# Optimization experiments

Hardware: AMD Instinct MI355X
Metric: run time of the kernel (lower is better)

Reference implementation:

```python
import jax, jax.numpy as jnp
import numpy as np


def _glorot(key, shape):
    fan_in, fan_out = shape[0], shape[1]
    lim = np.sqrt(6.0 / (fan_in + fan_out))
    return jax.random.uniform(key, shape, jnp.float32, -lim, lim)


def setup_inputs() -> dict:
    key = jax.random.key(0)
    ks = jax.random.split(key, 32)
    B, NR, NT = 16384, 64, 128
    inp = {
        "tier0_features": jax.random.normal(ks[0], (B, 44), jnp.float32),
        "robot_features": jax.random.normal(ks[1], (B, NR, 6), jnp.float32),
        "track_features": jax.random.normal(ks[2], (B, NT, 7), jnp.float32),
        # robot SetEncoder: 6 -> 64 -> 64 -> 32
        "rw1": _glorot(ks[3], (6, 64)),  "rb1": jnp.zeros((64,), jnp.float32),
        "rw2": _glorot(ks[4], (64, 64)), "rb2": jnp.zeros((64,), jnp.float32),
        "rw3": _glorot(ks[5], (64, 32)), "rb3": jnp.zeros((32,), jnp.float32),
        # track SetEncoder: 7 -> 64 -> 64 -> 32
        "tw1": _glorot(ks[6], (7, 64)),  "tb1": jnp.zeros((64,), jnp.float32),
        "tw2": _glorot(ks[7], (64, 64)), "tb2": jnp.zeros((64,), jnp.float32),
        "tw3": _glorot(ks[8], (64, 32)), "tb3": jnp.zeros((32,), jnp.float32),
        # head MLP: 108 -> 128 -> 128 -> 64 -> 1
        "mw1": _glorot(ks[9], (108, 128)),  "mb1": jnp.zeros((128,), jnp.float32),
        "mw2": _glorot(ks[10], (128, 128)), "mb2": jnp.zeros((128,), jnp.float32),
        "mw3": _glorot(ks[11], (128, 64)),  "mb3": jnp.zeros((64,), jnp.float32),
        "mw4": _glorot(ks[12], (64, 1)),    "mb4": jnp.zeros((1,), jnp.float32),
    }
    return inp


def _set_encode(x, w1, b1, w2, b2, w3, b3):
    # x: [B, N, d_in] -> pooled [B, 32]; mask=None path: mean+max over set dim
    h = jax.nn.relu(jnp.einsum('bnd,dh->bnh', x, w1) + b1)
    h = jax.nn.relu(jnp.einsum('bnh,hk->bnk', h, w2) + b2)
    e = jnp.einsum('bnk,ko->bno', h, w3) + b3
    return (e.mean(axis=1) + e.max(axis=1)) * 0.5


def reference(tier0_features, robot_features, track_features,
              rw1, rb1, rw2, rb2, rw3, rb3,
              tw1, tb1, tw2, tb2, tw3, tb3,
              mw1, mb1, mw2, mb2, mw3, mb3, mw4, mb4):
    robot_emb = _set_encode(robot_features, rw1, rb1, rw2, rb2, rw3, rb3)  # [B,32]
    track_emb = _set_encode(track_features, tw1, tb1, tw2, tb2, tw3, tb3)  # [B,32]
    c = jnp.concatenate([tier0_features, robot_emb, track_emb], axis=1)    # [B,108]
    h = jax.nn.relu(c @ mw1 + mb1)
    h = jax.nn.relu(h @ mw2 + mb2)
    h = jax.nn.relu(h @ mw3 + mb3)
    return (h @ mw4 + mb4).squeeze(-1)  # [B]
```

## Files before the change

kernel.cpp:

```cpp
#include <hip/hip_runtime.h>
#include <hip/hip_bf16.h>

#define DEV_INLINE __device__ __forceinline__

typedef __bf16 bf16x8 __attribute__((ext_vector_type(8)));
typedef float  floatx4 __attribute__((ext_vector_type(4)));

DEV_INLINE bf16x8 ld_frag(const __bf16* p) {
    union { uint4 u; bf16x8 v; } t;
    t.u = *(const uint4*)p;
    return t.v;
}
DEV_INLINE bf16x8 pack_relu2(floatx4 a, floatx4 b) {
    float2 p0 = {fmaxf(a[0], 0.0f), fmaxf(a[1], 0.0f)};
    float2 p1 = {fmaxf(a[2], 0.0f), fmaxf(a[3], 0.0f)};
    float2 p2 = {fmaxf(b[0], 0.0f), fmaxf(b[1], 0.0f)};
    float2 p3 = {fmaxf(b[2], 0.0f), fmaxf(b[3], 0.0f)};
    union { __hip_bfloat162 h[4]; bf16x8 v; } t;
    t.h[0] = __float22bfloat162_rn(p0);
    t.h[1] = __float22bfloat162_rn(p1);
    t.h[2] = __float22bfloat162_rn(p2);
    t.h[3] = __float22bfloat162_rn(p3);
    return t.v;
}
DEV_INLINE floatx4 vmax4(floatx4 a, floatx4 b) {
    floatx4 r;
#pragma unroll
    for (int i = 0; i < 4; ++i) r[i] = fmaxf(a[i], b[i]);
    return r;
}

template<int N, int Kp, int Ks>
DEV_INLINE void tp(__bf16* dst, const float* __restrict__ src, int idx0, int stride) {
    for (int e = idx0; e < N * Kp; e += stride) {
        int n = e / Kp, k = e - n * Kp;
        dst[e] = (k < Ks) ? (__bf16)src[k * N + n] : (__bf16)0.0f;
    }
}
template<int N, int Kp, int Ks>
DEV_INLINE void tp_b(__bf16* dst, const float* __restrict__ src,
                     const float* __restrict__ bias, int idx0, int stride) {
    for (int e = idx0; e < N * Kp; e += stride) {
        int n = e / Kp, k = e - n * Kp;
        float v = (k < Ks) ? src[k * N + n] : ((k == Ks) ? bias[n] : 0.0f);
        dst[e] = (__bf16)v;
    }
}
template<int N, int K>
DEV_INLINE void tp_perm(__bf16* dst, const float* __restrict__ src, int idx0, int stride) {
    for (int e = idx0; e < N * K; e += stride) {
        int n = e / K, kh = e - n * K;
        int qd = (kh >> 3) & 3, kq = kh >> 5, j = kh & 7;
        int c = (2 * kq + (j >> 2)) * 16 + qd * 4 + (j & 3);
        dst[e] = (__bf16)src[c * N + n];
    }
}

__global__ __launch_bounds__(256)
void prep_kernel(const float* __restrict__ rw1, const float* __restrict__ rb1,
                 const float* __restrict__ rw2, const float* __restrict__ rw3,
                 const float* __restrict__ tw1, const float* __restrict__ tb1,
                 const float* __restrict__ tw2, const float* __restrict__ tw3,
                 const float* __restrict__ mw1, const float* __restrict__ mw2,
                 const float* __restrict__ mw3, __bf16* __restrict__ wb)
{
    int i0 = blockIdx.x * 256 + threadIdx.x;
    int st = gridDim.x * 256;
    tp_b   < 64,  32,   6>(wb + 0,     rw1, rb1, i0, st);
    tp_perm< 64,  64>     (wb + 2048,  rw2, i0, st);
    tp_perm< 32,  64>     (wb + 6144,  rw3, i0, st);
    tp_b   < 64,  32,   7>(wb + 8192,  tw1, tb1, i0, st);
    tp_perm< 64,  64>     (wb + 10240, tw2, i0, st);
    tp_perm< 32,  64>     (wb + 14336, tw3, i0, st);
    tp     <128, 128, 108>(wb + 16384, mw1, i0, st);
    tp_perm<128, 128>     (wb + 32768, mw2, i0, st);
    tp_perm< 64, 128>     (wb + 49152, mw3, i0, st);
}

struct __align__(16) EncSmem {
    float2 pb[2 * 4 * 32];
    float  bs[64];
    __bf16 xs[2][128 * 8];
};

template<int DIN>
DEV_INLINE void x_load(const float* __restrict__ X, int bid, int tid, float (&g)[4]) {
    const float* src = X + (size_t)bid * 128 * DIN;
#pragma unroll
    for (int p = 0; p < 4; ++p) {
        int e = tid + p * 256;
        if ((DIN == 6) ? (p < 3) : (e < 128 * 7)) g[p] = src[e];
    }
}
template<int DIN>
DEV_INLINE void x_store(__bf16* xbuf, int tid, const float (&g)[4]) {
#pragma unroll
    for (int p = 0; p < 4; ++p) {
        int e = tid + p * 256;
        if ((DIN == 6) ? (p < 3) : (e < 128 * 7)) {
            int r = e / DIN, k = e - r * DIN;
            xbuf[r * 8 + k] = (__bf16)g[p];
        }
    }
}

template<int DIN, int S, int ITERS>
DEV_INLINE void enc_loop(EncSmem& sm, const float* __restrict__ X,
                         const __bf16* __restrict__ w1p,
                         const __bf16* __restrict__ w2p,
                         const __bf16* __restrict__ w3p,
                         const float* __restrict__ b2, const float* __restrict__ b3,
                         __bf16* __restrict__ out, int bid0)
{
    constexpr int NB = 128 / S;
    const int tid = threadIdx.x;
    const int w   = tid >> 6;
    const int l64 = tid & 63;
    const int ln  = l64 & 15;
    const int qd  = l64 >> 4;

    if (tid < 64) sm.bs[tid] = b2[tid];

    {
        __bf16* xf = &sm.xs[0][0];
        if (DIN == 6) {
            union { __bf16 h[2]; uint32_t u; } c;
            c.h[0] = (__bf16)1.0f; c.h[1] = (__bf16)0.0f;
            *(uint32_t*)&xf[tid * 8 + 6] = c.u;
        } else {
            xf[tid * 8 + 7] = (__bf16)1.0f;
        }
    }
    const float b3f = (tid < NB * 32) ? b3[tid & 31] : 0.0f;

    bf16x8 w1f[4], w2f[4][2], w3f[2][2];
#pragma unroll
    for (int mt = 0; mt < 4; ++mt)
        w1f[mt] = ld_frag(&w1p[(mt * 16 + ln) * 32 + qd * 8]);
#pragma unroll
    for (int mt = 0; mt < 4; ++mt)
#pragma unroll
        for (int kq = 0; kq < 2; ++kq)
            w2f[mt][kq] = ld_frag(&w2p[(mt * 16 + ln) * 64 + kq * 32 + qd * 8]);
#pragma unroll
    for (int mt = 0; mt < 2; ++mt)
#pragma unroll
        for (int kq = 0; kq < 2; ++kq)
            w3f[mt][kq] = ld_frag(&w3p[(mt * 16 + ln) * 64 + kq * 32 + qd * 8]);

    bf16x8 zf;
#pragma unroll
    for (int j = 0; j < 8; ++j) zf[j] = (__bf16)0.0f;
    const floatx4 z4 = {0.0f, 0.0f, 0.0f, 0.0f};

    float g[4];
    x_load<DIN>(X, bid0, tid, g);
    x_store<DIN>(sm.xs[0], tid, g);
    __syncthreads();

    int cur = 0, pbuf = 0;
    for (int it = 0; it < ITERS; ++it) {
        const int bid = bid0 + it;
        if (it + 1 < ITERS) x_load<DIN>(X, bid + 1, tid, g);

        bf16x8 xb[2];
#pragma unroll
        for (int t = 0; t < 2; ++t) {
            bf16x8 v = zf;
            if (qd == 0) {
                const int row = (2 * w + t) * 16 + ln;
                v = ld_frag(&sm.xs[cur][row * 8]);
            }
            xb[t] = v;
        }

        floatx4 a1[2][4];
#pragma unroll
        for (int mt = 0; mt < 4; ++mt)
#pragma unroll
            for (int t = 0; t < 2; ++t)
                a1[t][mt] = __builtin_amdgcn_mfma_f32_16x16x32_bf16(w1f[mt], xb[t], z4, 0, 0, 0);
        bf16x8 f1[2][2];
#pragma unroll
        for (int t = 0; t < 2; ++t)
#pragma unroll
            for (int kq = 0; kq < 2; ++kq)
                f1[t][kq] = pack_relu2(a1[t][2 * kq], a1[t][2 * kq + 1]);

        floatx4 a2[2][4];
#pragma unroll
        for (int mt = 0; mt < 4; ++mt) {
            floatx4 bv = *(const floatx4*)&sm.bs[mt * 16 + qd * 4];
#pragma unroll
            for (int t = 0; t < 2; ++t) {
                floatx4 acc;
                acc = __builtin_amdgcn_mfma_f32_16x16x32_bf16(w2f[mt][0], f1[t][0], bv, 0, 0, 0);
                acc = __builtin_amdgcn_mfma_f32_16x16x32_bf16(w2f[mt][1], f1[t][1], acc, 0, 0, 0);
                a2[t][mt] = acc;
            }
        }
        bf16x8 f2[2][2];
#pragma unroll
        for (int t = 0; t < 2; ++t)
#pragma unroll
            for (int kq = 0; kq < 2; ++kq)
                f2[t][kq] = pack_relu2(a2[t][2 * kq], a2[t][2 * kq + 1]);

        floatx4 a3[2][2];
#pragma unroll
        for (int mt = 0; mt < 2; ++mt)
#pragma unroll
            for (int t = 0; t < 2; ++t) {
                floatx4 acc;
                acc = __builtin_amdgcn_mfma_f32_16x16x32_bf16(f2[t][0], w3f[mt][0], z4, 0, 0, 0);
                acc = __builtin_amdgcn_mfma_f32_16x16x32_bf16(f2[t][1], w3f[mt][1], acc, 0, 0, 0);
                a3[t][mt] = acc;
            }

        float2 part[2];
#pragma unroll
        for (int mt = 0; mt < 2; ++mt) {
            floatx4 sv = a3[0][mt] + a3[1][mt];
            floatx4 mv = vmax4(a3[0][mt], a3[1][mt]);
            float s = (sv[0] + sv[1]) + (sv[2] + sv[3]);
            float m = fmaxf(fmaxf(mv[0], mv[1]), fmaxf(mv[2], mv[3]));
            s += __shfl_xor(s, 16); m = fmaxf(m, __shfl_xor(m, 16));
            s += __shfl_xor(s, 32); m = fmaxf(m, __shfl_xor(m, 32));
            part[mt] = make_float2(s, m);
        }

        if (it + 1 < ITERS) x_store<DIN>(sm.xs[cur ^ 1], tid, g);

        if (qd == 0) {
            sm.pb[pbuf * 128 + w * 32 + ln]      = part[0];
            sm.pb[pbuf * 128 + w * 32 + 16 + ln] = part[1];
        }
        __syncthreads();

        if (tid < NB * 32) {
            const int b = tid >> 5, f = tid & 31;
            constexpr int WPB = 4 / NB;
            float s = 0.0f, m = -3.4e38f;
#pragma unroll
            for (int wv = 0; wv < WPB; ++wv) {
                float2 v = sm.pb[pbuf * 128 + (b * WPB + wv) * 32 + f];
                s += v.x;
                m = fmaxf(m, v.y);
            }
            out[((size_t)bid * NB + b) * 32 + f] =
                (__bf16)(0.5f * (s * (1.0f / S) + m) + b3f);
        }
        cur ^= 1; pbuf ^= 1;
    }
}

__global__ __launch_bounds__(256, 4)
void enc_fused(const float* __restrict__ rX, const float* __restrict__ tX,
               const __bf16* __restrict__ wb,
               const float* __restrict__ rb2, const float* __restrict__ rb3,
               const float* __restrict__ tb2, const float* __restrict__ tb3,
               __bf16* __restrict__ remb, __bf16* __restrict__ temb)
{
    __shared__ EncSmem sm;
    if ((int)blockIdx.x < 1024)
        enc_loop<6, 64, 8>(sm, rX, wb, wb + 2048, wb + 6144,
                           rb2, rb3, remb, blockIdx.x * 8);
    else
        enc_loop<7, 128, 8>(sm, tX, wb + 8192, wb + 10240, wb + 14336,
                            tb2, tb3, temb, ((int)blockIdx.x - 1024) * 8);
}

__global__ __launch_bounds__(256)
void head_mfma(const float* __restrict__ t0,
               const __bf16* __restrict__ remb, const __bf16* __restrict__ temb,
               const __bf16* __restrict__ hw1, const float* __restrict__ b1,
               const __bf16* __restrict__ hw2, const float* __restrict__ b2,
               const __bf16* __restrict__ hw3, const float* __restrict__ b3,
               const float* __restrict__ w4, const float* __restrict__ b4,
               float* __restrict__ out)
{
    __shared__ __align__(16) __bf16 cb[64 * 136];

    const int tid = threadIdx.x;
    const int w   = tid >> 6;
    const int l64 = tid & 63;
    const int ln  = l64 & 15;
    const int qd  = l64 >> 4;
    const int g0  = blockIdx.x * 64;

    for (int i = tid; i < 64 * 44; i += 256) {
        int r = i / 44, k = i - r * 44;
        cb[r * 136 + k] = (__bf16)t0[(size_t)(g0 + r) * 44 + k];
    }
    for (int i = tid; i < 64 * 32; i += 256) {
        int r = i >> 5, k = i & 31;
        cb[r * 136 + 44 + k] = remb[(size_t)(g0 + r) * 32 + k];
        cb[r * 136 + 76 + k] = temb[(size_t)(g0 + r) * 32 + k];
    }
    for (int i = tid; i < 64 * 20; i += 256) {
        int r = i / 20, k = i - r * 20;
        cb[r * 136 + 108 + k] = (__bf16)0.0f;
    }
    __syncthreads();

    bf16x8 cf[4];
#pragma unroll
    for (int kq = 0; kq < 4; ++kq)
        cf[kq] = ld_frag(&cb[(w * 16 + ln) * 136 + kq * 32 + qd * 8]);
    floatx4 acc1[8];
#pragma unroll
    for (int mt = 0; mt < 8; ++mt) {
        float4 bv = *(const float4*)&b1[mt * 16 + qd * 4];
        floatx4 acc = (floatx4){bv.x, bv.y, bv.z, bv.w};
#pragma unroll
        for (int kq = 0; kq < 4; ++kq) {
            bf16x8 af = ld_frag(&hw1[(mt * 16 + ln) * 128 + kq * 32 + qd * 8]);
            acc = __builtin_amdgcn_mfma_f32_16x16x32_bf16(af, cf[kq], acc, 0, 0, 0);
        }
        acc1[mt] = acc;
    }
    bf16x8 f1[4];
#pragma unroll
    for (int kq = 0; kq < 4; ++kq)
        f1[kq] = pack_relu2(acc1[2 * kq], acc1[2 * kq + 1]);

    floatx4 acc2[8];
#pragma unroll
    for (int mt = 0; mt < 8; ++mt) {
        float4 bv = *(const float4*)&b2[mt * 16 + qd * 4];
        floatx4 acc = (floatx4){bv.x, bv.y, bv.z, bv.w};
#pragma unroll
        for (int kq = 0; kq < 4; ++kq) {
            bf16x8 af = ld_frag(&hw2[(mt * 16 + ln) * 128 + kq * 32 + qd * 8]);
            acc = __builtin_amdgcn_mfma_f32_16x16x32_bf16(af, f1[kq], acc, 0, 0, 0);
        }
        acc2[mt] = acc;
    }
    bf16x8 f2[4];
#pragma unroll
    for (int kq = 0; kq < 4; ++kq)
        f2[kq] = pack_relu2(acc2[2 * kq], acc2[2 * kq + 1]);

    floatx4 acc3[4];
#pragma unroll
    for (int mt = 0; mt < 4; ++mt) {
        float4 bv = *(const float4*)&b3[mt * 16 + qd * 4];
        floatx4 acc = (floatx4){bv.x, bv.y, bv.z, bv.w};
#pragma unroll
        for (int kq = 0; kq < 4; ++kq) {
            bf16x8 af = ld_frag(&hw3[(mt * 16 + ln) * 128 + kq * 32 + qd * 8]);
            acc = __builtin_amdgcn_mfma_f32_16x16x32_bf16(af, f2[kq], acc, 0, 0, 0);
        }
        acc3[mt] = acc;
    }

    float part = 0.0f;
#pragma unroll
    for (int mt = 0; mt < 4; ++mt) {
        float4 wv = *(const float4*)&w4[mt * 16 + qd * 4];
        part = fmaf(fmaxf(acc3[mt][0], 0.0f), wv.x, part);
        part = fmaf(fmaxf(acc3[mt][1], 0.0f), wv.y, part);
        part = fmaf(fmaxf(acc3[mt][2], 0.0f), wv.z, part);
        part = fmaf(fmaxf(acc3[mt][3], 0.0f), wv.w, part);
    }
    part += __shfl_xor(part, 16);
    part += __shfl_xor(part, 32);
    if (qd == 0)
        out[g0 + w * 16 + ln] = part + b4[0];
}

extern "C" void kernel_launch(void* const* d_in, const int* in_sizes, int n_in,
                              void* d_out, int out_size, void* d_ws, size_t ws_size,
                              hipStream_t stream)
{
    const float* t0  = (const float*)d_in[0];
    const float* rX  = (const float*)d_in[1];
    const float* tX  = (const float*)d_in[2];
    const float* rw1 = (const float*)d_in[3];  const float* rb1 = (const float*)d_in[4];
    const float* rw2 = (const float*)d_in[5];  const float* rb2 = (const float*)d_in[6];
    const float* rw3 = (const float*)d_in[7];  const float* rb3 = (const float*)d_in[8];
    const float* tw1 = (const float*)d_in[9];  const float* tb1 = (const float*)d_in[10];
    const float* tw2 = (const float*)d_in[11]; const float* tb2 = (const float*)d_in[12];
    const float* tw3 = (const float*)d_in[13]; const float* tb3 = (const float*)d_in[14];
    const float* mw1 = (const float*)d_in[15]; const float* mb1 = (const float*)d_in[16];
    const float* mw2 = (const float*)d_in[17]; const float* mb2 = (const float*)d_in[18];
    const float* mw3 = (const float*)d_in[19]; const float* mb3 = (const float*)d_in[20];
    const float* mw4 = (const float*)d_in[21]; const float* mb4 = (const float*)d_in[22];
    float* out = (float*)d_out;

    const int B = 16384;
    __bf16* remb = (__bf16*)d_ws;
    __bf16* temb = (__bf16*)((char*)d_ws + ((size_t)1 << 20));
    __bf16* wb   = (__bf16*)((char*)d_ws + ((size_t)2 << 20));
    const __bf16* mw1b = wb + 16384; const __bf16* mw2b = wb + 32768;
    const __bf16* mw3b = wb + 49152;

    prep_kernel<<<64, 256, 0, stream>>>(rw1, rb1, rw2, rw3, tw1, tb1, tw2, tw3,
                                        mw1, mw2, mw3, wb);
    enc_fused<<<3072, 256, 0, stream>>>(rX, tX, wb,
                                        rb2, rb3, tb2, tb3,
                                        remb, temb);
    head_mfma<<<B / 64, 256, 0, stream>>>(t0, remb, temb,
                                          mw1b, mb1, mw2b, mb2, mw3b, mb3,
                                          mw4, mb4, out);
}
```

Before: 226.3 us.

## Stage encoder weights in swizzled LDS instead of registers, raise occupancy

Each encoder block now copies its 16KB of packed bf16 weights into shared memory, using an XOR swizzle on the 64-wide matrices, and reloads MFMA fragments from LDS every iteration instead of keeping them in VGPRs. The second layer is restructured to compute and pack in pairs of row tiles, which shortens live ranges. Launch bounds are raised from 4 to 6 blocks per SIMD. The aim is to cut register pressure so more waves are resident and hide latency, at the cost of extra LDS reads per iteration and more shared memory per block, which could itself cap occupancy.

Measured after the change: 211.6 us. 6.5% less time.

```diff
diff --git a/kernel.cpp b/kernel.cpp
--- a/kernel.cpp
+++ b/kernel.cpp
@@ -78,7 +78,8 @@
 }
 
 struct __align__(16) EncSmem {
-    float2 pb[2 * 4 * 32];
+    __bf16 wt[8192];
+    float2 pb[2 * 128];
     float  bs[64];
     __bf16 xs[2][128 * 8];
 };
@@ -106,9 +107,7 @@
 
 template<int DIN, int S, int ITERS>
 DEV_INLINE void enc_loop(EncSmem& sm, const float* __restrict__ X,
-                         const __bf16* __restrict__ w1p,
-                         const __bf16* __restrict__ w2p,
-                         const __bf16* __restrict__ w3p,
+                         const __bf16* __restrict__ wsrc,
                          const float* __restrict__ b2, const float* __restrict__ b3,
                          __bf16* __restrict__ out, int bid0)
 {
@@ -121,6 +120,14 @@
 
     if (tid < 64) sm.bs[tid] = b2[tid];
 
+    for (int c = tid; c < 1024; c += 256) {
+        uint4 v = *(const uint4*)(wsrc + c * 8);
+        int byte = c * 16;
+        int dst  = (c < 256) ? byte
+                             : (byte ^ (((byte >> 7) & 7) << 4));
+        *(uint4*)((char*)sm.wt + dst) = v;
+    }
+
     {
         __bf16* xf = &sm.xs[0][0];
         if (DIN == 6) {
@@ -133,20 +140,10 @@
     }
     const float b3f = (tid < NB * 32) ? b3[tid & 31] : 0.0f;
 
-    bf16x8 w1f[4], w2f[4][2], w3f[2][2];
-#pragma unroll
-    for (int mt = 0; mt < 4; ++mt)
-        w1f[mt] = ld_frag(&w1p[(mt * 16 + ln) * 32 + qd * 8]);
-#pragma unroll
-    for (int mt = 0; mt < 4; ++mt)
-#pragma unroll
-        for (int kq = 0; kq < 2; ++kq)
-            w2f[mt][kq] = ld_frag(&w2p[(mt * 16 + ln) * 64 + kq * 32 + qd * 8]);
-#pragma unroll
-    for (int mt = 0; mt < 2; ++mt)
-#pragma unroll
-        for (int kq = 0; kq < 2; ++kq)
-            w3f[mt][kq] = ld_frag(&w3p[(mt * 16 + ln) * 64 + kq * 32 + qd * 8]);
+    const int wb1   = (ln * 32 + qd * 8) * 2;
+    const int wb64a = ((ln * 64 + qd * 8) * 2)       ^ ((ln & 7) << 4);
+    const int wb64b = ((ln * 64 + 32 + qd * 8) * 2)  ^ ((ln & 7) << 4);
+    const char* wtb = (const char*)sm.wt;
 
     bf16x8 zf;
 #pragma unroll
@@ -176,10 +173,12 @@
 
         floatx4 a1[2][4];
 #pragma unroll
-        for (int mt = 0; mt < 4; ++mt)
+        for (int mt = 0; mt < 4; ++mt) {
+            bf16x8 wf = ld_frag((const __bf16*)(wtb + wb1 + mt * 1024));
 #pragma unroll
             for (int t = 0; t < 2; ++t)
-                a1[t][mt] = __builtin_amdgcn_mfma_f32_16x16x32_bf16(w1f[mt], xb[t], z4, 0, 0, 0);
+                a1[t][mt] = __builtin_amdgcn_mfma_f32_16x16x32_bf16(wf, xb[t], z4, 0, 0, 0);
+        }
         bf16x8 f1[2][2];
 #pragma unroll
         for (int t = 0; t < 2; ++t)
@@ -187,35 +186,42 @@
             for (int kq = 0; kq < 2; ++kq)
                 f1[t][kq] = pack_relu2(a1[t][2 * kq], a1[t][2 * kq + 1]);
 
-        floatx4 a2[2][4];
-#pragma unroll
-        for (int mt = 0; mt < 4; ++mt) {
-            floatx4 bv = *(const floatx4*)&sm.bs[mt * 16 + qd * 4];
+        bf16x8 f2[2][2];
+#pragma unroll
+        for (int pr = 0; pr < 2; ++pr) {
+            floatx4 a2[2][2];
+#pragma unroll
+            for (int m = 0; m < 2; ++m) {
+                const int mt = pr * 2 + m;
+                floatx4 bv = *(const floatx4*)&sm.bs[mt * 16 + qd * 4];
+                bf16x8 wf0 = ld_frag((const __bf16*)(wtb + 4096 + mt * 2048 + wb64a));
+                bf16x8 wf1 = ld_frag((const __bf16*)(wtb + 4096 + mt * 2048 + wb64b));
+#pragma unroll
+                for (int t = 0; t < 2; ++t) {
+                    floatx4 acc;
+                    acc = __builtin_amdgcn_mfma_f32_16x16x32_bf16(wf0, f1[t][0], bv, 0, 0, 0);
+                    acc = __builtin_amdgcn_mfma_f32_16x16x32_bf16(wf1, f1[t][1], acc, 0, 0, 0);
+                    a2[t][m] = acc;
+                }
+            }
+#pragma unroll
+            for (int t = 0; t < 2; ++t)
+                f2[t][pr] = pack_relu2(a2[t][0], a2[t][1]);
+        }
+
+        floatx4 a3[2][2];
+#pragma unroll
+        for (int mt = 0; mt < 2; ++mt) {
+            bf16x8 wf0 = ld_frag((const __bf16*)(wtb + 12288 + mt * 2048 + wb64a));
+            bf16x8 wf1 = ld_frag((const __bf16*)(wtb + 12288 + mt * 2048 + wb64b));
 #pragma unroll
             for (int t = 0; t < 2; ++t) {
                 floatx4 acc;
-                acc = __builtin_amdgcn_mfma_f32_16x16x32_bf16(w2f[mt][0], f1[t][0], bv, 0, 0, 0);
-                acc = __builtin_amdgcn_mfma_f32_16x16x32_bf16(w2f[mt][1], f1[t][1], acc, 0, 0, 0);
-                a2[t][mt] = acc;
-            }
-        }
-        bf16x8 f2[2][2];
-#pragma unroll
-        for (int t = 0; t < 2; ++t)
-#pragma unroll
-            for (int kq = 0; kq < 2; ++kq)
-                f2[t][kq] = pack_relu2(a2[t][2 * kq], a2[t][2 * kq + 1]);
-
-        floatx4 a3[2][2];
-#pragma unroll
-        for (int mt = 0; mt < 2; ++mt)
-#pragma unroll
-            for (int t = 0; t < 2; ++t) {
-                floatx4 acc;
-                acc = __builtin_amdgcn_mfma_f32_16x16x32_bf16(f2[t][0], w3f[mt][0], z4, 0, 0, 0);
-                acc = __builtin_amdgcn_mfma_f32_16x16x32_bf16(f2[t][1], w3f[mt][1], acc, 0, 0, 0);
+                acc = __builtin_amdgcn_mfma_f32_16x16x32_bf16(f2[t][0], wf0, z4, 0, 0, 0);
+                acc = __builtin_amdgcn_mfma_f32_16x16x32_bf16(f2[t][1], wf1, acc, 0, 0, 0);
                 a3[t][mt] = acc;
             }
+        }
 
         float2 part[2];
 #pragma unroll
@@ -254,7 +260,7 @@
     }
 }
 
-__global__ __launch_bounds__(256, 4)
+__global__ __launch_bounds__(256, 6)
 void enc_fused(const float* __restrict__ rX, const float* __restrict__ tX,
                const __bf16* __restrict__ wb,
                const float* __restrict__ rb2, const float* __restrict__ rb3,
@@ -263,11 +269,10 @@
 {
     __shared__ EncSmem sm;
     if ((int)blockIdx.x < 1024)
-        enc_loop<6, 64, 8>(sm, rX, wb, wb + 2048, wb + 6144,
-                           rb2, rb3, remb, blockIdx.x * 8);
+        enc_loop<6, 64, 8>(sm, rX, wb, rb2, rb3, remb, blockIdx.x * 8);
     else
-        enc_loop<7, 128, 8>(sm, tX, wb + 8192, wb + 10240, wb + 14336,
-                            tb2, tb3, temb, ((int)blockIdx.x - 1024) * 8);
+        enc_loop<7, 128, 8>(sm, tX, wb + 8192, tb2, tb3, temb,
+                            ((int)blockIdx.x - 1024) * 8);
 }
 
 __global__ __launch_bounds__(256)
```
